# Kernel optimization log

Measured on AMD Instinct MI355X. Metric: run time of the kernel, lower is better.

Reference implementation:

```python
import jax, jax.numpy as jnp
import numpy as np

H = W = M = 16          # 3D token grid
N = H * W * M           # 4096 tokens
D = 256                 # dims == out_dim == key/value dim == x1_dim
HC = 8                  # head_count
D2 = 2 * D              # concat width
C2 = 4 * D              # MixFFN hidden
OUT = D                 # out_dim
UP = OUT // 2           # PatchExpand output channels
B = 4


def _ln(x, g, b, eps=1e-5):
    m = jnp.mean(x, axis=-1, keepdims=True)
    v = jnp.mean(jnp.square(x - m), axis=-1, keepdims=True)
    return (x - m) / jnp.sqrt(v + eps) * g + b


def setup_inputs() -> dict:
    key = jax.random.key(0)
    ks = jax.random.split(key, 16)
    s = 0.02
    inp = {
        "x1": jax.random.normal(ks[0], (B, N, D), jnp.float32),
        "x2": jax.random.normal(ks[1], (B, N, D), jnp.float32),
        # x1_linear (x1_dim -> out_dim)
        "w_x1": s * jax.random.normal(ks[2], (D, OUT), jnp.float32),
        "b_x1": jnp.zeros((OUT,), jnp.float32),
        # CrossAttentionBlock.norm1 (shared for x1 and x2)
        "g_n1": jnp.ones((D,), jnp.float32),
        "be_n1": jnp.zeros((D,), jnp.float32),
        # Cross_Attention.reprojection: 1x1x1 Conv3d D -> 2D == channel matmul
        "w_rep": s * jax.random.normal(ks[3], (D, D2), jnp.float32),
        "b_rep": jnp.zeros((D2,), jnp.float32),
        # Cross_Attention.norm (LayerNorm 2D)
        "g_an": jnp.ones((D2,), jnp.float32),
        "be_an": jnp.zeros((D2,), jnp.float32),
        # CrossAttentionBlock.norm2 (LayerNorm 2D)
        "g_n2": jnp.ones((D2,), jnp.float32),
        "be_n2": jnp.zeros((D2,), jnp.float32),
        # MixFFN_skip fc1 (2D -> 4D), depthwise conv3d, norm1, fc2
        "w_fc1": s * jax.random.normal(ks[4], (D2, C2), jnp.float32),
        "b_fc1": jnp.zeros((C2,), jnp.float32),
        "w_dw": s * jax.random.normal(ks[5], (C2, 1, 3, 3, 3), jnp.float32),
        "b_dw": jnp.zeros((C2,), jnp.float32),
        "g_m1": jnp.ones((C2,), jnp.float32),
        "be_m1": jnp.zeros((C2,), jnp.float32),
        "w_fc2": s * jax.random.normal(ks[6], (C2, D2), jnp.float32),
        "b_fc2": jnp.zeros((D2,), jnp.float32),
        # concat_linear (2*dims -> out_dim)
        "w_cat": s * jax.random.normal(ks[7], (D2, OUT), jnp.float32),
        "b_cat": jnp.zeros((OUT,), jnp.float32),
        # PatchExpand: expand (out_dim -> 4*out_dim, no bias) + LayerNorm(out_dim//2)
        "w_exp": s * jax.random.normal(ks[8], (OUT, 4 * OUT), jnp.float32),
        "g_up": jnp.ones((UP,), jnp.float32),
        "be_up": jnp.zeros((UP,), jnp.float32),
    }
    return inp


def reference(x1, x2, w_x1, b_x1, g_n1, be_n1, w_rep, b_rep, g_an, be_an,
              g_n2, be_n2, w_fc1, b_fc1, w_dw, b_dw, g_m1, be_m1,
              w_fc2, b_fc2, w_cat, b_cat, w_exp, g_up, be_up):
    b = x1.shape[0]
    hk = D // HC  # head key channels (== head value channels here)

    # x1_linear
    x1e = x1 @ w_x1 + b_x1                                 # [B,N,D]

    # shared norm1 applied to both streams
    n1 = _ln(x1e, g_n1, be_n1)
    n2 = _ln(x2, g_n1, be_n1)

    # Cross_Attention (efficient attention, softmax-normalized K/Q)
    kq = jnp.transpose(n2, (0, 2, 1)).reshape(b, HC, hk, N)   # keys==queries
    val = jnp.transpose(n1, (0, 2, 1)).reshape(b, HC, hk, N)
    k = jax.nn.softmax(kq, axis=3)          # softmax over tokens
    q = jax.nn.softmax(kq, axis=2)          # softmax over head channels
    ctx = jnp.einsum('bhkn,bhvn->bhkv', k, val)        # [B,HC,hk,hv]
    att = jnp.einsum('bhkv,bhkn->bhvn', ctx, q)        # [B,HC,hv,N]
    att = att.reshape(b, D, N)                          # concat heads
    # 1x1x1 Conv3d reprojection D -> 2D, then to [B,N,2D] + LayerNorm
    rep = jnp.einsum('bdn,de->bne', att, w_rep) + b_rep
    rep = _ln(rep, g_an, be_an)                         # [B,N,2D]

    # residual concat + attention
    tx = jnp.concatenate([x1e, x2], axis=2) + rep       # [B,N,2D]

    # MixFFN_skip
    h = _ln(tx, g_n2, be_n2) @ w_fc1 + b_fc1            # [B,N,C2]
    hv = jnp.transpose(h, (0, 2, 1)).reshape(b, C2, H, W, M)
    dw = jax.lax.conv_general_dilated(
        hv, w_dw, window_strides=(1, 1, 1), padding='SAME',
        feature_group_count=C2,
        dimension_numbers=('NCDHW', 'OIDHW', 'NCDHW'))
    dw = dw + b_dw[None, :, None, None, None]
    dw = jnp.transpose(dw.reshape(b, C2, N), (0, 2, 1))  # [B,N,C2]
    ax = jax.nn.gelu(_ln(dw + h, g_m1, be_m1), approximate=False)
    mx = tx + (ax @ w_fc2 + b_fc2)                       # [B,N,2D]

    # concat_linear
    y = mx @ w_cat + b_cat                               # [B,N,OUT]

    ye = y @ w_exp                                       # [B,N,4*OUT]
    ye = ye.reshape(b, 8 * N, UP)                        # view+reshape of contiguous
    out = _ln(ye, g_up, be_up)                           # [B,8N,OUT//2]
    return out
```

## Files before the change

kernel.cpp:

```cpp
#include <hip/hip_runtime.h>
#include <math.h>

using u16 = unsigned short;
typedef __bf16 bf16x8 __attribute__((ext_vector_type(8)));
typedef float f32x4 __attribute__((ext_vector_type(4)));

#define BB 4
#define NN 4096
#define DD 256
#define DD2 512
#define CC2 1024
static constexpr int ROWS = BB * NN;
static constexpr size_t MB = 1024 * 1024;

__device__ __forceinline__ u16 f2bf(float f) {
  union { float f; unsigned u; } v; v.f = f;
  unsigned r = v.u + 0x7fffu + ((v.u >> 16) & 1u);
  return (u16)(r >> 16);
}
__device__ __forceinline__ float bf2f(u16 u) {
  union { unsigned u; float f; } v; v.u = ((unsigned)u) << 16;
  return v.f;
}
__device__ __forceinline__ float u2f(unsigned x) {
  union { unsigned u; float f; } v; v.u = x; return v.f;
}

__global__ __launch_bounds__(256) void wprep_all(
    const float* __restrict__ w_x1, const float* __restrict__ w_rep,
    const float* __restrict__ w_fc1, const float* __restrict__ w_fc2,
    const float* __restrict__ w_cat, const float* __restrict__ w_exp,
    const float* __restrict__ w_dw,
    u16* __restrict__ w_x1t, u16* __restrict__ w_rept,
    u16* __restrict__ w_fc1t, u16* __restrict__ w_fc2t,
    u16* __restrict__ w_catt, u16* __restrict__ w_expt,
    float* __restrict__ w_dwt) {
  int i = blockIdx.x * 256 + threadIdx.x;
  if (i < 65536) { int n = i >> 8, k = i & 255; w_x1t[i] = f2bf(w_x1[k * 256 + n]); return; }
  i -= 65536;
  if (i < 131072) { int n = i >> 8, k = i & 255; w_rept[i] = f2bf(w_rep[k * 512 + n]); return; }
  i -= 131072;
  if (i < 524288) { int n = i >> 9, k = i & 511; w_fc1t[i] = f2bf(w_fc1[k * 1024 + n]); return; }
  i -= 524288;
  if (i < 524288) { int n = i >> 10, k = i & 1023; w_fc2t[i] = f2bf(w_fc2[k * 512 + n]); return; }
  i -= 524288;
  if (i < 131072) { int n = i >> 9, k = i & 511; w_catt[i] = f2bf(w_cat[k * 256 + n]); return; }
  i -= 131072;
  if (i < 262144) { int n = i >> 8, k = i & 255; w_expt[i] = f2bf(w_exp[k * 1024 + n]); return; }
  i -= 262144;
  if (i < 27648) { int widx = i >> 10, c = i & 1023; w_dwt[i] = w_dw[c * 27 + widx]; }
}

template <int K, int EPI, bool AF32 = false>
__global__ __launch_bounds__(256, 2) void gemm_mfma(
    const u16* __restrict__ A, const u16* __restrict__ Bt,
    const float* __restrict__ bias, const u16* __restrict__ resid,
    void* __restrict__ Cout, int nTilesN,
    const float* __restrict__ gup, const float* __restrict__ beup) {
  const int t = threadIdx.x;
  const int m0 = (blockIdx.x / nTilesN) * 128;
  const int n0 = (blockIdx.x % nTilesN) * 128;
  const int Ncols = nTilesN * 128;
  const int lane = t & 63, wid = t >> 6;
  const int wr = wid >> 1, wc = wid & 1;
  const int lrow = lane & 15, kgrp = lane >> 4;

  __shared__ u16 ldsA[2][128 * 32];
  __shared__ u16 ldsB[2][128 * 32];

  int srow[2], sslot[2];
#pragma unroll
  for (int c = 0; c < 2; ++c) {
    int idx = c * 256 + t;
    srow[c] = idx >> 2;
    sslot[c] = (idx & 3) ^ ((srow[c] >> 1) & 3);
  }

  int offA[4], offB[4];
#pragma unroll
  for (int m = 0; m < 4; ++m) {
    int r = wr * 64 + m * 16 + lrow;
    offA[m] = r * 32 + ((kgrp ^ ((r >> 1) & 3)) * 8);
  }
#pragma unroll
  for (int n = 0; n < 4; ++n) {
    int r = wc * 64 + n * 16 + lrow;
    offB[n] = r * 32 + ((kgrp ^ ((r >> 1) & 3)) * 8);
  }

  f32x4 acc[4][4];
#pragma unroll
  for (int m = 0; m < 4; ++m)
#pragma unroll
    for (int n = 0; n < 4; ++n) acc[m][n] = f32x4{0.f, 0.f, 0.f, 0.f};

  auto loadA = [&](int c, int kc) -> uint4 {
    if constexpr (AF32) {
      const float* A32 = (const float*)A;
      const float* p = A32 + (size_t)(m0 + srow[c]) * K + kc + sslot[c] * 8;
      float4 f0 = *(const float4*)p;
      float4 f1 = *(const float4*)(p + 4);
      u16 o[8] = {f2bf(f0.x), f2bf(f0.y), f2bf(f0.z), f2bf(f0.w),
                  f2bf(f1.x), f2bf(f1.y), f2bf(f1.z), f2bf(f1.w)};
      return *(uint4*)o;
    } else {
      return *(const uint4*)(A + (size_t)(m0 + srow[c]) * K + kc + sslot[c] * 8);
    }
  };

  uint4 ra[2], rb[2];
#pragma unroll
  for (int c = 0; c < 2; ++c) {
    ra[c] = loadA(c, 0);
    rb[c] = *(const uint4*)(Bt + (size_t)(n0 + srow[c]) * K + sslot[c] * 8);
  }
#pragma unroll
  for (int c = 0; c < 2; ++c) {
    int idx = c * 256 + t;
    *(uint4*)&ldsA[0][idx * 8] = ra[c];
    *(uint4*)&ldsB[0][idx * 8] = rb[c];
  }
  __syncthreads();

  const int nt = K / 32;
  for (int tt = 0; tt < nt; ++tt) {
    const int cur = tt & 1;
    if (tt + 1 < nt) {
      const int kc = (tt + 1) * 32;
#pragma unroll
      for (int c = 0; c < 2; ++c) {
        ra[c] = loadA(c, kc);
        rb[c] = *(const uint4*)(Bt + (size_t)(n0 + srow[c]) * K + kc + sslot[c] * 8);
      }
    }
    bf16x8 af[4], bf[4];
#pragma unroll
    for (int m = 0; m < 4; ++m) af[m] = *(const bf16x8*)&ldsA[cur][offA[m]];
#pragma unroll
    for (int n = 0; n < 4; ++n) bf[n] = *(const bf16x8*)&ldsB[cur][offB[n]];
#pragma unroll
    for (int m = 0; m < 4; ++m)
#pragma unroll
      for (int n = 0; n < 4; ++n)
        acc[m][n] = __builtin_amdgcn_mfma_f32_16x16x32_bf16(af[m], bf[n], acc[m][n], 0, 0, 0);
    if (tt + 1 < nt) {
#pragma unroll
      for (int c = 0; c < 2; ++c) {
        int idx = c * 256 + t;
        *(uint4*)&ldsA[cur ^ 1][idx * 8] = ra[c];
        *(uint4*)&ldsB[cur ^ 1][idx * 8] = rb[c];
      }
    }
    __syncthreads();
  }

  if (EPI == 3) {
    __shared__ float lnS[2][128], lnQ[2][128];
    float s_[4][4], q_[4][4];
#pragma unroll
    for (int m = 0; m < 4; ++m)
#pragma unroll
      for (int j = 0; j < 4; ++j) {
        float s = 0.f, q = 0.f;
#pragma unroll
        for (int n = 0; n < 4; ++n) {
          float v = acc[m][n][j];
          s += v; q += v * v;
        }
        s_[m][j] = s; q_[m][j] = q;
      }
#pragma unroll
    for (int msk = 1; msk < 16; msk <<= 1) {
#pragma unroll
      for (int m = 0; m < 4; ++m)
#pragma unroll
        for (int j = 0; j < 4; ++j) {
          s_[m][j] += __shfl_xor(s_[m][j], msk, 64);
          q_[m][j] += __shfl_xor(q_[m][j], msk, 64);
        }
    }
    if (lrow == 0) {
#pragma unroll
      for (int m = 0; m < 4; ++m)
#pragma unroll
        for (int j = 0; j < 4; ++j) {
          int r = wr * 64 + m * 16 + kgrp * 4 + j;
          lnS[wc][r] = s_[m][j];
          lnQ[wc][r] = q_[m][j];
        }
    }
    __syncthreads();
#pragma unroll
    for (int m = 0; m < 4; ++m) {
      const int rb0 = wr * 64 + m * 16 + kgrp * 4;
#pragma unroll
      for (int j = 0; j < 4; ++j) {
        const int r = rb0 + j;
        float S = lnS[0][r] + lnS[1][r];
        float Q = lnQ[0][r] + lnQ[1][r];
        float mean = S * (1.0f / 128.0f);
        float var = Q * (1.0f / 128.0f) - mean * mean;
        float iv = rsqrtf(var + 1e-5f);
#pragma unroll
        for (int n = 0; n < 4; ++n) {
          int lc = wc * 64 + n * 16 + lrow;
          ((float*)Cout)[(size_t)(m0 + r) * Ncols + n0 + lc] =
              (acc[m][n][j] - mean) * iv * gup[lc] + beup[lc];
        }
      }
    }
    return;
  }

  float bcol[4];
#pragma unroll
  for (int n = 0; n < 4; ++n) {
    int col = n0 + wc * 64 + n * 16 + (lane & 15);
    bcol[n] = bias ? bias[col] : 0.f;
  }
#pragma unroll
  for (int m = 0; m < 4; ++m) {
    const int r0 = m0 + wr * 64 + m * 16 + kgrp * 4;
#pragma unroll
    for (int n = 0; n < 4; ++n) {
      const int col = n0 + wc * 64 + n * 16 + (lane & 15);
#pragma unroll
      for (int j = 0; j < 4; ++j) {
        float v = acc[m][n][j] + bcol[n];
        size_t idx = (size_t)(r0 + j) * Ncols + col;
        if (EPI == 0) {
          ((float*)Cout)[idx] = v;
        } else if (EPI == 1) {
          ((u16*)Cout)[idx] = f2bf(v);
        } else {
          v += bf2f(resid[idx]);
          ((u16*)Cout)[idx] = f2bf(v);
        }
      }
    }
  }
}

template <bool INBF, bool ROWOUT, bool TOUT>
__global__ __launch_bounds__(256) void ln256x(const void* __restrict__ in,
                                              const float* __restrict__ g,
                                              const float* __restrict__ be,
                                              u16* __restrict__ rowout,
                                              u16* __restrict__ tout) {
  const int row = blockIdx.x, t = threadIdx.x;
  __shared__ float ws[8];
  float v;
  if (INBF) v = bf2f(((const u16*)in)[(size_t)row * DD + t]);
  else v = ((const float*)in)[(size_t)row * DD + t];
  float s = v, q = v * v;
#pragma unroll
  for (int m = 1; m < 64; m <<= 1) {
    s += __shfl_xor(s, m, 64);
    q += __shfl_xor(q, m, 64);
  }
  if ((t & 63) == 0) { ws[t >> 6] = s; ws[4 + (t >> 6)] = q; }
  __syncthreads();
  s = ws[0] + ws[1] + ws[2] + ws[3];
  q = ws[4] + ws[5] + ws[6] + ws[7];
  float mean = s * (1.0f / DD);
  float var = q * (1.0f / DD) - mean * mean;
  float iv = rsqrtf(var + 1e-5f);
  u16 rb = f2bf((v - mean) * iv * g[t] + be[t]);
  if (ROWOUT) rowout[(size_t)row * DD + t] = rb;
  if (TOUT) {
    int b = row >> 12, n = row & 4095;
    tout[((size_t)(b * 256 + t)) * 4096 + n] = rb;
  }
}

__global__ __launch_bounds__(256) void k34_ctx(
    const u16* __restrict__ n2T, const u16* __restrict__ n1T,
    float* __restrict__ ctx) {
  const int bid = blockIdx.x;
  const int bx = (bid & 7) * 128 + (bid >> 3);
  const int b = bx >> 8, d = bx & 255;
  const int h = d >> 5, kk = d & 31;
  const int t = threadIdx.x;
  __shared__ u16 prow[4096];
  __shared__ float xred[8];
  __shared__ float sw[128];
  const u16* src = n2T + (size_t)bx * 4096;
  ((uint4*)prow)[t] = ((const uint4*)src)[t];
  ((uint4*)prow)[256 + t] = ((const uint4*)src)[256 + t];
  __syncthreads();
  float mx = -1e30f;
#pragma unroll
  for (int i = 0; i < 16; ++i) mx = fmaxf(mx, bf2f(prow[i * 256 + t]));
#pragma unroll
  for (int m = 1; m < 64; m <<= 1) mx = fmaxf(mx, __shfl_xor(mx, m, 64));
  if ((t & 63) == 0) xred[t >> 6] = mx;
  __syncthreads();
  mx = fmaxf(fmaxf(xred[0], xred[1]), fmaxf(xred[2], xred[3]));
  float sme = 0.f;
#pragma unroll
  for (int i = 0; i < 16; ++i) sme += __expf(bf2f(prow[i * 256 + t]) - mx);
#pragma unroll
  for (int m = 1; m < 64; m <<= 1) sme += __shfl_xor(sme, m, 64);
  if ((t & 63) == 0) xred[4 + (t >> 6)] = sme;
  __syncthreads();
  const float inv = 1.0f / (xred[4] + xred[5] + xred[6] + xred[7]);

  float acc[32];
#pragma unroll
  for (int v = 0; v < 32; ++v) acc[v] = 0.f;
  const u16* vbase = n1T + ((size_t)(b * 256 + h * 32)) * 4096;
  for (int i = 0; i < 16; ++i) {
    const int n = i * 256 + t;
    const float p = __expf(bf2f(prow[n]) - mx) * inv;
#pragma unroll
    for (int v = 0; v < 32; ++v)
      acc[v] += p * bf2f(vbase[(size_t)v * 4096 + n]);
  }
#pragma unroll
  for (int v = 0; v < 32; ++v) {
#pragma unroll
    for (int m = 1; m < 64; m <<= 1) acc[v] += __shfl_xor(acc[v], m, 64);
  }
  if ((t & 63) == 0) {
#pragma unroll
    for (int v = 0; v < 32; ++v) sw[(t >> 6) * 32 + v] = acc[v];
  }
  __syncthreads();
  if (t < 32)
    ctx[(((size_t)(b * 8 + h)) * 32 + kk) * 32 + t] =
        sw[t] + sw[32 + t] + sw[64 + t] + sw[96 + t];
}

__global__ __launch_bounds__(256) void k5_attT(
    const u16* __restrict__ n2, const float* __restrict__ ctx,
    u16* __restrict__ attT) {
  const int row = blockIdx.x, t = threadIdx.x;
  const int b = row >> 12;
  const int h = t >> 5, v = t & 31;
  __shared__ float nr[DD];
  __shared__ float q[DD];
  nr[t] = bf2f(n2[(size_t)row * DD + t]);
  __syncthreads();
  float mx = -1e30f;
  for (int c = 0; c < 32; ++c) mx = fmaxf(mx, nr[h * 32 + c]);
  float sm = 0.f;
  for (int c = 0; c < 32; ++c) sm += __expf(nr[h * 32 + c] - mx);
  q[t] = __expf(nr[t] - mx) / sm;
  __syncthreads();
  const float* cb = ctx + ((size_t)(b * 8 + h) * 32) * 32 + v;
  float acc = 0.f;
#pragma unroll
  for (int k = 0; k < 32; ++k) acc += cb[k * 32] * q[h * 32 + k];
  attT[(size_t)row * DD + t] = f2bf(acc);
}

__global__ __launch_bounds__(256) void l3_reptx(
    const u16* __restrict__ rep_b, const u16* __restrict__ x1e,
    const float* __restrict__ x2,
    const float* __restrict__ g_an, const float* __restrict__ be_an,
    const float* __restrict__ g_n2, const float* __restrict__ be_n2,
    u16* __restrict__ tx, u16* __restrict__ txln) {
  const int row = blockIdx.x, t = threadIdx.x;
  __shared__ float ws[8];
  float a0 = bf2f(rep_b[(size_t)row * DD2 + t]);
  float a1 = bf2f(rep_b[(size_t)row * DD2 + 256 + t]);
  float s = a0 + a1, q = a0 * a0 + a1 * a1;
#pragma unroll
  for (int m = 1; m < 64; m <<= 1) {
    s += __shfl_xor(s, m, 64);
    q += __shfl_xor(q, m, 64);
  }
  if ((t & 63) == 0) { ws[t >> 6] = s; ws[4 + (t >> 6)] = q; }
  __syncthreads();
  s = ws[0] + ws[1] + ws[2] + ws[3];
  q = ws[4] + ws[5] + ws[6] + ws[7];
  float mean = s * (1.0f / DD2);
  float var = q * (1.0f / DD2) - mean * mean;
  float iv = rsqrtf(var + 1e-5f);
  float r0 = (a0 - mean) * iv * g_an[t] + be_an[t];
  float r1 = (a1 - mean) * iv * g_an[256 + t] + be_an[256 + t];
  float t0 = bf2f(x1e[(size_t)row * DD + t]) + r0;
  float t1 = x2[(size_t)row * DD + t] + r1;
  tx[(size_t)row * DD2 + t] = f2bf(t0);
  tx[(size_t)row * DD2 + 256 + t] = f2bf(t1);
  __syncthreads();
  s = t0 + t1; q = t0 * t0 + t1 * t1;
#pragma unroll
  for (int m = 1; m < 64; m <<= 1) {
    s += __shfl_xor(s, m, 64);
    q += __shfl_xor(q, m, 64);
  }
  if ((t & 63) == 0) { ws[t >> 6] = s; ws[4 + (t >> 6)] = q; }
  __syncthreads();
  s = ws[0] + ws[1] + ws[2] + ws[3];
  q = ws[4] + ws[5] + ws[6] + ws[7];
  mean = s * (1.0f / DD2);
  var = q * (1.0f / DD2) - mean * mean;
  iv = rsqrtf(var + 1e-5f);
  txln[(size_t)row * DD2 + t] = f2bf((t0 - mean) * iv * g_n2[t] + be_n2[t]);
  txln[(size_t)row * DD2 + 256 + t] = f2bf((t1 - mean) * iv * g_n2[256 + t] + be_n2[256 + t]);
}

__global__ __launch_bounds__(1024) void c8a_col(
    const u16* __restrict__ h, const float* __restrict__ w_dwt,
    const float* __restrict__ b_dw, const float* __restrict__ g,
    const float* __restrict__ be, u16* __restrict__ ax) {
  const int bid = blockIdx.x;
  const int cidx = (bid & 7) * 128 + (bid >> 3);
  const int b = cidx >> 8, y = (cidx >> 4) & 15, x = cidx & 15;
  const int t = threadIdx.x;
  const int lane = t & 63, wave = t >> 6;
  const size_t hb = (size_t)b * NN * CC2;

  __shared__ float2 red[16][16];
  __shared__ float2 stats[16];

  int coln[9];
  float cmask[9];
#pragma unroll
  for (int dy = -1; dy <= 1; ++dy)
#pragma unroll
    for (int dx = -1; dx <= 1; ++dx) {
      int qq = (dy + 1) * 3 + (dx + 1);
      int yy = y + dy, xx = x + dx;
      bool ok = ((unsigned)yy < 16u) && ((unsigned)xx < 16u);
      coln[qq] = ((ok ? yy : y) << 4) | (ok ? xx : x);
      cmask[qq] = ok ? 1.f : 0.f;
    }

  float wr[3][9];
#pragma unroll
  for (int p = 0; p < 3; ++p)
#pragma unroll
    for (int qq = 0; qq < 9; ++qq)
      wr[p][qq] = w_dwt[(p * 9 + qq) * CC2 + t] * cmask[qq];
  const float bias = b_dw[t];

  u16 win[3][9];
#define LOADPLANE(ZL, SLOT)                                                   \
  do {                                                                        \
    if ((ZL) >= 0 && (ZL) < 16) {                                             \
      _Pragma("unroll") for (int qq = 0; qq < 9; ++qq) win[SLOT][qq] =        \
          h[hb + (size_t)((((ZL) << 8) | coln[qq])) * CC2 + t];               \
    } else {                                                                  \
      _Pragma("unroll") for (int qq = 0; qq < 9; ++qq) win[SLOT][qq] = 0;     \
    }                                                                         \
  } while (0)

  LOADPLANE(-1, 0);
  LOADPLANE(0, 1);
  LOADPLANE(1, 2);

  float vs[16];
#pragma unroll
  for (int z = 0; z < 16; ++z) {
    const int pm1 = z % 3, pz = (z + 1) % 3, pp1 = (z + 2) % 3;
    float a0 = bias;
#pragma unroll
    for (int qq = 0; qq < 9; ++qq) {
      a0 += bf2f(win[pm1][qq]) * wr[0][qq];
      a0 += bf2f(win[pz][qq]) * wr[1][qq];
      a0 += bf2f(win[pp1][qq]) * wr[2][qq];
    }
    float v = a0 + bf2f(win[pz][4]);
    LOADPLANE(z + 2, pm1);
    vs[z] = v;
    float s = v, q2 = v * v;
#pragma unroll
    for (int m = 1; m < 64; m <<= 1) {
      s += __shfl_xor(s, m, 64);
      q2 += __shfl_xor(q2, m, 64);
    }
    if (lane == 0) red[z][wave] = make_float2(s, q2);
  }
#undef LOADPLANE
  __syncthreads();

  {
    const int z = wave;
    float S = (lane < 16) ? red[z][lane].x : 0.f;
    float Q = (lane < 16) ? red[z][lane].y : 0.f;
#pragma unroll
    for (int m = 1; m < 16; m <<= 1) {
      S += __shfl_xor(S, m, 64);
      Q += __shfl_xor(Q, m, 64);
    }
    if (lane == 0) {
      float mean = S * (1.0f / CC2);
      float var = Q * (1.0f / CC2) - mean * mean;
      stats[z] = make_float2(mean, rsqrtf(var + 1e-5f));
    }
  }
  __syncthreads();

  const float gg = g[t], bb = be[t];
#pragma unroll
  for (int z = 0; z < 16; ++z) {
    float2 st = stats[z];
    float u = (vs[z] - st.x) * st.y * gg + bb;
    float s2 = 1.5957691216f * (u + 0.044715f * u * u * u);
    float o = u / (1.0f + __expf(-s2));
    ax[((size_t)(b * NN + ((z << 8) | (y << 4) | x))) * CC2 + t] = f2bf(o);
  }
}

extern "C" void kernel_launch(void* const* d_in, const int* in_sizes, int n_in,
                              void* d_out, int out_size, void* d_ws, size_t ws_size,
                              hipStream_t stream) {
  const float* x1    = (const float*)d_in[0];
  const float* x2    = (const float*)d_in[1];
  const float* w_x1  = (const float*)d_in[2];
  const float* b_x1  = (const float*)d_in[3];
  const float* g_n1  = (const float*)d_in[4];
  const float* be_n1 = (const float*)d_in[5];
  const float* w_rep = (const float*)d_in[6];
  const float* b_rep = (const float*)d_in[7];
  const float* g_an  = (const float*)d_in[8];
  const float* be_an = (const float*)d_in[9];
  const float* g_n2  = (const float*)d_in[10];
  const float* be_n2 = (const float*)d_in[11];
  const float* w_fc1 = (const float*)d_in[12];
  const float* b_fc1 = (const float*)d_in[13];
  const float* w_dw  = (const float*)d_in[14];
  const float* b_dw  = (const float*)d_in[15];
  const float* g_m1  = (const float*)d_in[16];
  const float* be_m1 = (const float*)d_in[17];
  const float* w_fc2 = (const float*)d_in[18];
  const float* b_fc2 = (const float*)d_in[19];
  const float* w_cat = (const float*)d_in[20];
  const float* b_cat = (const float*)d_in[21];
  const float* w_exp = (const float*)d_in[22];
  const float* g_up  = (const float*)d_in[23];
  const float* be_up = (const float*)d_in[24];

  char* ws = (char*)d_ws;
  float* out = (float*)d_out;

  u16*   x1e_b   = (u16*)(ws + 8 * MB);
  u16*   n1T     = (u16*)(ws + 24 * MB);
  u16*   n2b     = (u16*)(ws + 32 * MB);
  u16*   n2T     = (u16*)(ws + 40 * MB);
  float* ctx     = (float*)(ws + 48 * MB);
  u16*   rep_b   = (u16*)(ws + 49 * MB);
  u16*   tx      = (u16*)(ws + 81 * MB);
  u16*   txln    = (u16*)(ws + 97 * MB);
  u16*   hbuf    = (u16*)(ws + 113 * MB);
  u16*   attT    = (u16*)(ws + 0);
  u16*   ax      = (u16*)(ws + 49 * MB);
  u16*   mx      = (u16*)(ws + 8 * MB);
  u16*   ybuf    = (u16*)(ws + 0);
  u16*   w_x1t   = (u16*)(ws + 145 * MB);
  u16*   w_rept  = w_x1t + 256 * 256;
  u16*   w_fc1t  = w_rept + 512 * 256;
  u16*   w_fc2t  = w_fc1t + 1024 * 512;
  u16*   w_catt  = w_fc2t + 512 * 1024;
  u16*   w_expt  = w_catt + 256 * 512;
  float* w_dwt   = (float*)(ws + 149 * MB);

  wprep_all<<<(1666048 + 255) / 256, 256, 0, stream>>>(
      w_x1, w_rep, w_fc1, w_fc2, w_cat, w_exp, w_dw,
      w_x1t, w_rept, w_fc1t, w_fc2t, w_catt, w_expt, w_dwt);

  gemm_mfma<256, 1, true><<<(ROWS / 128) * 2, 256, 0, stream>>>(
      (const u16*)x1, w_x1t, b_x1, nullptr, x1e_b, 2, nullptr, nullptr);
  ln256x<true, false, true><<<ROWS, 256, 0, stream>>>(x1e_b, g_n1, be_n1, nullptr, n1T);
  ln256x<false, true, true><<<ROWS, 256, 0, stream>>>(x2, g_n1, be_n1, n2b, n2T);
  k34_ctx<<<BB * 256, 256, 0, stream>>>(n2T, n1T, ctx);
  k5_attT<<<ROWS, 256, 0, stream>>>(n2b, ctx, attT);
  gemm_mfma<256, 1><<<(ROWS / 128) * 4, 256, 0, stream>>>(
      attT, w_rept, b_rep, nullptr, rep_b, 4, nullptr, nullptr);
  l3_reptx<<<ROWS, 256, 0, stream>>>(rep_b, x1e_b, x2, g_an, be_an, g_n2, be_n2, tx, txln);
  gemm_mfma<512, 1><<<(ROWS / 128) * 8, 256, 0, stream>>>(
      txln, w_fc1t, b_fc1, nullptr, hbuf, 8, nullptr, nullptr);
  c8a_col<<<1024, 1024, 0, stream>>>(hbuf, w_dwt, b_dw, g_m1, be_m1, ax);
  gemm_mfma<1024, 2><<<(ROWS / 128) * 4, 256, 0, stream>>>(
      ax, w_fc2t, b_fc2, tx, mx, 4, nullptr, nullptr);
  gemm_mfma<512, 1><<<(ROWS / 128) * 2, 256, 0, stream>>>(
      mx, w_catt, b_cat, nullptr, ybuf, 2, nullptr, nullptr);
  gemm_mfma<256, 3><<<(ROWS / 128) * 8, 256, 0, stream>>>(
      ybuf, w_expt, nullptr, nullptr, out, 8, g_up, be_up);
}
```

Measured before the change: 323.9 us.

## Use direct global-to-LDS async loads in bf16 GEMMs and merge LayerNorm launches

For the bf16-input GEMM variants, the register-staged global loads and LDS stores are replaced with global_load_lds builtins that write tiles straight into shared memory. This removes the register round trip and the separate LDS write phase. The two per-row LayerNorm launches are also merged into one kernel with a doubled grid, saving one launch. The async path relies on the existing single __syncthreads per iteration to cover completion of the direct LDS loads, which is a correctness risk if the wait is not inserted.

```diff
diff --git a/kernel.cpp b/kernel.cpp
--- a/kernel.cpp
+++ b/kernel.cpp
@@ -24,6 +24,11 @@
 }
 __device__ __forceinline__ float u2f(unsigned x) {
   union { unsigned u; float f; } v; v.u = x; return v.f;
+}
+__device__ __forceinline__ void gload16(const void* g, void* l) {
+  __builtin_amdgcn_global_load_lds(
+      (const __attribute__((address_space(1))) void*)g,
+      (__attribute__((address_space(3))) void*)l, 16, 0, 0);
 }
 
 __global__ __launch_bounds__(256) void wprep_all(
@@ -94,31 +99,40 @@
 #pragma unroll
     for (int n = 0; n < 4; ++n) acc[m][n] = f32x4{0.f, 0.f, 0.f, 0.f};
 
-  auto loadA = [&](int c, int kc) -> uint4 {
-    if constexpr (AF32) {
-      const float* A32 = (const float*)A;
-      const float* p = A32 + (size_t)(m0 + srow[c]) * K + kc + sslot[c] * 8;
-      float4 f0 = *(const float4*)p;
-      float4 f1 = *(const float4*)(p + 4);
-      u16 o[8] = {f2bf(f0.x), f2bf(f0.y), f2bf(f0.z), f2bf(f0.w),
-                  f2bf(f1.x), f2bf(f1.y), f2bf(f1.z), f2bf(f1.w)};
-      return *(uint4*)o;
-    } else {
-      return *(const uint4*)(A + (size_t)(m0 + srow[c]) * K + kc + sslot[c] * 8);
-    }
+  auto loadA32 = [&](int c, int kc) -> uint4 {
+    const float* A32 = (const float*)A;
+    const float* p = A32 + (size_t)(m0 + srow[c]) * K + kc + sslot[c] * 8;
+    float4 f0 = *(const float4*)p;
+    float4 f1 = *(const float4*)(p + 4);
+    u16 o[8] = {f2bf(f0.x), f2bf(f0.y), f2bf(f0.z), f2bf(f0.w),
+                f2bf(f1.x), f2bf(f1.y), f2bf(f1.z), f2bf(f1.w)};
+    return *(uint4*)o;
   };
+  auto stage_async = [&](int buf, int kc) {
+#pragma unroll
+    for (int c = 0; c < 2; ++c) {
+      gload16(A + (size_t)(m0 + srow[c]) * K + kc + sslot[c] * 8,
+              &ldsA[buf][(c * 256 + t) * 8]);
+      gload16(Bt + (size_t)(n0 + srow[c]) * K + kc + sslot[c] * 8,
+              &ldsB[buf][(c * 256 + t) * 8]);
+    }
+  };
 
   uint4 ra[2], rb[2];
-#pragma unroll
-  for (int c = 0; c < 2; ++c) {
-    ra[c] = loadA(c, 0);
-    rb[c] = *(const uint4*)(Bt + (size_t)(n0 + srow[c]) * K + sslot[c] * 8);
-  }
-#pragma unroll
-  for (int c = 0; c < 2; ++c) {
-    int idx = c * 256 + t;
-    *(uint4*)&ldsA[0][idx * 8] = ra[c];
-    *(uint4*)&ldsB[0][idx * 8] = rb[c];
+  if constexpr (AF32) {
+#pragma unroll
+    for (int c = 0; c < 2; ++c) {
+      ra[c] = loadA32(c, 0);
+      rb[c] = *(const uint4*)(Bt + (size_t)(n0 + srow[c]) * K + sslot[c] * 8);
+    }
+#pragma unroll
+    for (int c = 0; c < 2; ++c) {
+      int idx = c * 256 + t;
+      *(uint4*)&ldsA[0][idx * 8] = ra[c];
+      *(uint4*)&ldsB[0][idx * 8] = rb[c];
+    }
+  } else {
+    stage_async(0, 0);
   }
   __syncthreads();
 
@@ -127,10 +141,14 @@
     const int cur = tt & 1;
     if (tt + 1 < nt) {
       const int kc = (tt + 1) * 32;
-#pragma unroll
-      for (int c = 0; c < 2; ++c) {
-        ra[c] = loadA(c, kc);
-        rb[c] = *(const uint4*)(Bt + (size_t)(n0 + srow[c]) * K + kc + sslot[c] * 8);
+      if constexpr (AF32) {
+#pragma unroll
+        for (int c = 0; c < 2; ++c) {
+          ra[c] = loadA32(c, kc);
+          rb[c] = *(const uint4*)(Bt + (size_t)(n0 + srow[c]) * K + kc + sslot[c] * 8);
+        }
+      } else {
+        stage_async(cur ^ 1, kc);
       }
     }
     bf16x8 af[4], bf[4];
@@ -143,7 +161,7 @@
 #pragma unroll
       for (int n = 0; n < 4; ++n)
         acc[m][n] = __builtin_amdgcn_mfma_f32_16x16x32_bf16(af[m], bf[n], acc[m][n], 0, 0, 0);
-    if (tt + 1 < nt) {
+    if (AF32 && tt + 1 < nt) {
 #pragma unroll
       for (int c = 0; c < 2; ++c) {
         int idx = c * 256 + t;
@@ -241,17 +259,17 @@
   }
 }
 
-template <bool INBF, bool ROWOUT, bool TOUT>
-__global__ __launch_bounds__(256) void ln256x(const void* __restrict__ in,
-                                              const float* __restrict__ g,
-                                              const float* __restrict__ be,
-                                              u16* __restrict__ rowout,
-                                              u16* __restrict__ tout) {
-  const int row = blockIdx.x, t = threadIdx.x;
+__global__ __launch_bounds__(256) void ln256_both(
+    const u16* __restrict__ x1e_b, const float* __restrict__ x2,
+    const float* __restrict__ g, const float* __restrict__ be,
+    u16* __restrict__ n1T, u16* __restrict__ n2b, u16* __restrict__ n2T) {
+  int row = blockIdx.x;
+  const int t = threadIdx.x;
+  const bool first = row < ROWS;
+  if (!first) row -= ROWS;
   __shared__ float ws[8];
-  float v;
-  if (INBF) v = bf2f(((const u16*)in)[(size_t)row * DD + t]);
-  else v = ((const float*)in)[(size_t)row * DD + t];
+  float v = first ? bf2f(x1e_b[(size_t)row * DD + t])
+                  : x2[(size_t)row * DD + t];
   float s = v, q = v * v;
 #pragma unroll
   for (int m = 1; m < 64; m <<= 1) {
@@ -266,10 +284,12 @@
   float var = q * (1.0f / DD) - mean * mean;
   float iv = rsqrtf(var + 1e-5f);
   u16 rb = f2bf((v - mean) * iv * g[t] + be[t]);
-  if (ROWOUT) rowout[(size_t)row * DD + t] = rb;
-  if (TOUT) {
-    int b = row >> 12, n = row & 4095;
-    tout[((size_t)(b * 256 + t)) * 4096 + n] = rb;
+  int b = row >> 12, n = row & 4095;
+  if (first) {
+    n1T[((size_t)(b * 256 + t)) * 4096 + n] = rb;
+  } else {
+    n2b[(size_t)row * DD + t] = rb;
+    n2T[((size_t)(b * 256 + t)) * 4096 + n] = rb;
   }
 }
 
@@ -563,8 +583,7 @@
 
   gemm_mfma<256, 1, true><<<(ROWS / 128) * 2, 256, 0, stream>>>(
       (const u16*)x1, w_x1t, b_x1, nullptr, x1e_b, 2, nullptr, nullptr);
-  ln256x<true, false, true><<<ROWS, 256, 0, stream>>>(x1e_b, g_n1, be_n1, nullptr, n1T);
-  ln256x<false, true, true><<<ROWS, 256, 0, stream>>>(x2, g_n1, be_n1, n2b, n2T);
+  ln256_both<<<2 * ROWS, 256, 0, stream>>>(x1e_b, x2, g_n1, be_n1, n1T, n2b, n2T);
   k34_ctx<<<BB * 256, 256, 0, stream>>>(n2T, n1T, ctx);
   k5_attT<<<ROWS, 256, 0, stream>>>(n2b, ctx, attT);
   gemm_mfma<256, 1><<<(ROWS / 128) * 4, 256, 0, stream>>>(
```

Result: no change. 320.3 us (-1.1%).
